# Optimization experiments

Measured on AMD Instinct MI355X. Metric: run time of the kernel, lower is better.

## Reference

```python
import jax, jax.numpy as jnp
import numpy as np

B, LI, LJ, D = 32, 512, 512, 512
NN_DIM = 256  # agg output dim = 2*NN_DIM = 512


def setup_inputs() -> dict:
    key = jax.random.key(0)
    k1, k2, k3 = jax.random.split(key, 3)
    i = jax.random.normal(k1, (B, LI, D), dtype=jnp.float32)
    j = jax.random.normal(k2, (B, LJ, D), dtype=jnp.float32)
    W_agg = jax.random.normal(k3, (D, 2 * NN_DIM), dtype=jnp.float32) * (1.0 / np.sqrt(D))
    b_agg = jnp.zeros((2 * NN_DIM,), dtype=jnp.float32)
    return {"i": i, "j": j, "W_agg": W_agg, "b_agg": b_agg}


def _agg(x, W, b):
    # shared aggregation net: Dense(2*nn_dim) + tanh, then mean-pool over time
    # x: [B, L, D] -> [B, 2*nn_dim]
    return jnp.mean(jnp.tanh(jnp.einsum('bld,dh->blh', x, W) + b), axis=1)


def reference(i, j, W_agg, b_agg):
    # cross-attention scores: [B, Li, Lj]
    weight = jnp.einsum('bik,bjk->bij', i, j)
    # row softmax (over Lj) -> weights to aggregate j per i-position
    weight_j = jax.nn.softmax(weight, axis=2)
    # column softmax (over Li) -> weights to aggregate i per j-position
    weight_i = jax.nn.softmax(weight, axis=1)
    weighted_i = jnp.einsum('bij,bid->bjd', weight_i, i)  # [B, Lj, D]
    weighted_j = jnp.einsum('bij,bjd->bid', weight_j, j)  # [B, Li, D]
    output_i = jnp.abs(i - weighted_j)  # [B, Li, D]
    output_j = jnp.abs(j - weighted_i)  # [B, Lj, D]
    oi = _agg(output_i, W_agg, b_agg)   # [B, 2*nn_dim]
    oj = _agg(output_j, W_agg, b_agg)   # [B, 2*nn_dim]
    # K.mean(K.stack([oi, oj], axis=1), axis=1)
    return 0.5 * (oi + oj)
```

## Files before the change

kernel.cpp:

```cpp
#include <hip/hip_runtime.h>
#include <math.h>

#define B_ 32
#define L_ 512
#define D_ 512
#define H_ 512

typedef unsigned short u16;
typedef _Float16 h16;
typedef h16 half8 __attribute__((ext_vector_type(8)));
typedef float f32x4 __attribute__((ext_vector_type(4)));

#define SW(r, c) ((c) ^ (((r) >> 1) & 3))

typedef __attribute__((address_space(1))) void gvoid;
typedef __attribute__((address_space(3))) void svoid;
__device__ __forceinline__ void async_cp16(const void* g, void* l) {
    __builtin_amdgcn_global_load_lds((gvoid*)g, (svoid*)l, 16, 0, 0);
}

__device__ __forceinline__ u16 f2h(float x) {
    h16 h = (h16)x;
    u16 r;
    __builtin_memcpy(&r, &h, 2);
    return r;
}
__device__ __forceinline__ float h2f(u16 u) {
    h16 h;
    __builtin_memcpy(&h, &u, 2);
    return (float)h;
}

__device__ __forceinline__ void xcd_decode(int n, int& z, int& tile) {
    int xcd = n & 7, w = n >> 3;
    z = xcd + 8 * (w >> 4);
    tile = w & 15;
}

__global__ __launch_bounds__(256) void cvt_all(const float* __restrict__ I,
                                               const float* __restrict__ Jm,
                                               const float* __restrict__ W,
                                               u16* __restrict__ Ih, u16* __restrict__ IhT,
                                               u16* __restrict__ Jh, u16* __restrict__ JhT,
                                               u16* __restrict__ WT,
                                               float* __restrict__ out) {
    const int z = blockIdx.z;
    const float* src;
    u16* h;
    u16* hT;
    size_t base;
    if (z < 32) {
        src = I; h = Ih; hT = IhT; base = (size_t)z * 512 * 512;
    } else if (z < 64) {
        src = Jm; h = Jh; hT = JhT; base = (size_t)(z - 32) * 512 * 512;
    } else {
        src = W; h = nullptr; hT = WT; base = 0;
        out[(blockIdx.y * 8 + blockIdx.x) * 256 + threadIdx.x] = 0.0f;
    }
    const int r0 = blockIdx.y * 64, c0 = blockIdx.x * 64;
    __shared__ u16 t[64][66];
    const int tid = threadIdx.x;
    const int tr = tid >> 4, tc4 = (tid & 15) * 4;
#pragma unroll
    for (int rep = 0; rep < 4; ++rep) {
        int r = rep * 16 + tr;
        f32x4 v = *(const f32x4*)(src + base + (size_t)(r0 + r) * 512 + c0 + tc4);
        unsigned h0 = f2h(v[0]), h1 = f2h(v[1]), h2 = f2h(v[2]), h3 = f2h(v[3]);
        if (h)
            *(uint2*)(h + base + (size_t)(r0 + r) * 512 + c0 + tc4) =
                make_uint2(h0 | (h1 << 16), h2 | (h3 << 16));
        t[r][tc4] = (u16)h0; t[r][tc4 + 1] = (u16)h1;
        t[r][tc4 + 2] = (u16)h2; t[r][tc4 + 3] = (u16)h3;
    }
    __syncthreads();
#pragma unroll
    for (int rep = 0; rep < 4; ++rep) {
        int r = rep * 16 + tr;
        unsigned a = t[tc4][r], b = t[tc4 + 1][r], c = t[tc4 + 2][r], d = t[tc4 + 3][r];
        *(uint2*)(hT + base + (size_t)(c0 + r) * 512 + r0 + tc4) =
            make_uint2(a | (b << 16), c | (d << 16));
    }
}

__global__ __launch_bounds__(256, 2) void score_mfma(const u16* __restrict__ Ih,
                                                     const u16* __restrict__ Jh,
                                                     u16* __restrict__ P_un,
                                                     u16* __restrict__ P_unT,
                                                     float* __restrict__ rtmax,
                                                     float* __restrict__ rtsum,
                                                     float* __restrict__ ctmax,
                                                     float* __restrict__ ctsum) {
    int b, tile;
    xcd_decode(blockIdx.x, b, tile);
    const int i0 = (tile >> 2) * 128, j0 = (tile & 3) * 128;
    __shared__ u16 Ah[128 * 32], Bh[128 * 32];
    const int tid = threadIdx.x;
    const int wave = tid >> 6, lane = tid & 63;
    const int wm = (wave >> 1) * 64, wn = (wave & 1) * 64;
    const int lr = lane & 15, q = lane >> 4;
    const size_t boff = (size_t)b * L_ * D_;
    const u16* Ibh = Ih + boff;
    const u16* Jbh = Jh + boff;

    f32x4 acc[4][4] = {};

    for (int k0 = 0; k0 < D_; k0 += 32) {
#pragma unroll
        for (int h = 0; h < 2; ++h) {
            int g = wave * 2 + h;
            int r = g * 16 + (lane >> 2);
            int cg = SW(r, lane & 3);
            async_cp16(Ibh + (size_t)(i0 + r) * D_ + k0 + cg * 8, (char*)Ah + g * 1024);
            async_cp16(Jbh + (size_t)(j0 + r) * D_ + k0 + cg * 8, (char*)Bh + g * 1024);
        }
        __syncthreads();
        half8 af[4], bf[4];
#pragma unroll
        for (int mi = 0; mi < 4; ++mi) {
            int r = wm + mi * 16 + lr;
            af[mi] = *(const half8*)&Ah[r * 32 + SW(r, q) * 8];
        }
#pragma unroll
        for (int ni = 0; ni < 4; ++ni) {
            int r = wn + ni * 16 + lr;
            bf[ni] = *(const half8*)&Bh[r * 32 + SW(r, q) * 8];
        }
#pragma unroll
        for (int mi = 0; mi < 4; ++mi)
#pragma unroll
            for (int ni = 0; ni < 4; ++ni)
                acc[mi][ni] = __builtin_amdgcn_mfma_f32_16x16x32_f16(af[mi], bf[ni], acc[mi][ni], 0, 0, 0);
        __syncthreads();
    }

    float rm[4][4];
#pragma unroll
    for (int mi = 0; mi < 4; ++mi)
#pragma unroll
        for (int r4 = 0; r4 < 4; ++r4) {
            float t = fmaxf(fmaxf(acc[mi][0][r4], acc[mi][1][r4]),
                            fmaxf(acc[mi][2][r4], acc[mi][3][r4]));
#pragma unroll
            for (int off = 1; off < 16; off <<= 1) t = fmaxf(t, __shfl_xor(t, off));
            rm[mi][r4] = t;
        }
    float cm[4];
#pragma unroll
    for (int ni = 0; ni < 4; ++ni) {
        float u = -1e30f;
#pragma unroll
        for (int mi = 0; mi < 4; ++mi)
#pragma unroll
            for (int r4 = 0; r4 < 4; ++r4) u = fmaxf(u, acc[mi][ni][r4]);
        u = fmaxf(u, __shfl_xor(u, 16));
        u = fmaxf(u, __shfl_xor(u, 32));
        cm[ni] = u;
    }

    u16* Pu_b = P_un + (size_t)b * L_ * L_;
    u16* PuT_b = P_unT + (size_t)b * L_ * L_;
    float rs[4][4] = {};
    float cs[4] = {};
#pragma unroll
    for (int mi = 0; mi < 4; ++mi)
#pragma unroll
        for (int ni = 0; ni < 4; ++ni) {
            int i_base = i0 + wm + mi * 16 + q * 4;
            int j = j0 + wn + ni * 16 + lr;
            unsigned pc[4];
#pragma unroll
            for (int r4 = 0; r4 < 4; ++r4) {
                float er = __expf(acc[mi][ni][r4] - rm[mi][r4]);
                rs[mi][r4] += er;
                Pu_b[(size_t)(i_base + r4) * L_ + j] = f2h(er);
                float ec = __expf(acc[mi][ni][r4] - cm[ni]);
                cs[ni] += ec;
                pc[r4] = f2h(ec);
            }
            *(uint2*)&PuT_b[(size_t)j * L_ + i_base] =
                make_uint2(pc[0] | (pc[1] << 16), pc[2] | (pc[3] << 16));
        }

    const int gr = (j0 + wn) >> 6;
    const int gc = (i0 + wm) >> 6;
#pragma unroll
    for (int mi = 0; mi < 4; ++mi)
#pragma unroll
        for (int r4 = 0; r4 < 4; ++r4) {
            float s = rs[mi][r4];
#pragma unroll
            for (int off = 1; off < 16; off <<= 1) s += __shfl_xor(s, off);
            if (lr == 0) {
                int i = i0 + wm + mi * 16 + q * 4 + r4;
                rtmax[((size_t)b * L_ + i) * 8 + gr] = rm[mi][r4];
                rtsum[((size_t)b * L_ + i) * 8 + gr] = s;
            }
        }
#pragma unroll
    for (int ni = 0; ni < 4; ++ni) {
        float s = cs[ni];
        s += __shfl_xor(s, 16);
        s += __shfl_xor(s, 32);
        if (q == 0) {
            int j = j0 + wn + ni * 16 + lr;
            ctmax[((size_t)b * L_ + j) * 8 + gc] = cm[ni];
            ctsum[((size_t)b * L_ + j) * 8 + gc] = s;
        }
    }
}

__global__ __launch_bounds__(256, 2) void absdiff_scaled(const u16* __restrict__ P_un,
                                                         const u16* __restrict__ P_unT,
                                                         const float* __restrict__ rtmax,
                                                         const float* __restrict__ rtsum,
                                                         const float* __restrict__ ctmax,
                                                         const float* __restrict__ ctsum,
                                                         const u16* __restrict__ JhT,
                                                         const u16* __restrict__ IhT,
                                                         const u16* __restrict__ Ih,
                                                         const u16* __restrict__ Jh,
                                                         u16* __restrict__ Xall) {
    int zz, tile;
    xcd_decode(blockIdx.x, zz, tile);
    const int side = zz >> 5, b = zz & 31;
    const int a0 = (tile >> 2) * 128, d0 = (tile & 3) * 128;
    const u16* Pb = (side ? P_unT : P_un) + (size_t)b * L_ * L_;
    const float* tmax = (side ? ctmax : rtmax) + (size_t)b * L_ * 8;
    const float* tsum = (side ? ctsum : rtsum) + (size_t)b * L_ * 8;
    const u16* Vt = (side ? IhT : JhT) + (size_t)b * D_ * L_;
    const u16* Oh = (side ? Jh : Ih) + (size_t)b * L_ * D_;
    u16* Xb = Xall + (size_t)zz * L_ * D_;

    __shared__ u16 As[128 * 32], Bs[128 * 32];
    __shared__ float sc[128][8];
    const int tid = threadIdx.x;
    const int wave = tid >> 6, lane = tid & 63;
    const int wm = (wave >> 1) * 64, wn = (wave & 1) * 64;
    const int lr = lane & 15, q = lane >> 4;

    if (tid < 128) {
        const float* tm = tmax + (size_t)(a0 + tid) * 8;
        const float* ts = tsum + (size_t)(a0 + tid) * 8;
        f32x4 m0 = *(const f32x4*)tm, m1 = *(const f32x4*)(tm + 4);
        f32x4 s0 = *(const f32x4*)ts, s1 = *(const f32x4*)(ts + 4);
        float m = fmaxf(fmaxf(fmaxf(m0[0], m0[1]), fmaxf(m0[2], m0[3])),
                        fmaxf(fmaxf(m1[0], m1[1]), fmaxf(m1[2], m1[3])));
        float e0 = __expf(m0[0] - m), e1 = __expf(m0[1] - m);
        float e2 = __expf(m0[2] - m), e3 = __expf(m0[3] - m);
        float e4 = __expf(m1[0] - m), e5 = __expf(m1[1] - m);
        float e6 = __expf(m1[2] - m), e7 = __expf(m1[3] - m);
        float inv = 1.0f / (e0 * s0[0] + e1 * s0[1] + e2 * s0[2] + e3 * s0[3] +
                            e4 * s1[0] + e5 * s1[1] + e6 * s1[2] + e7 * s1[3]);
        sc[tid][0] = e0 * inv; sc[tid][1] = e1 * inv;
        sc[tid][2] = e2 * inv; sc[tid][3] = e3 * inv;
        sc[tid][4] = e4 * inv; sc[tid][5] = e5 * inv;
        sc[tid][6] = e6 * inv; sc[tid][7] = e7 * inv;
    }
    __syncthreads();

    f32x4 acc[4][4] = {};

    for (int k0 = 0; k0 < L_; k0 += 32) {
#pragma unroll
        for (int h = 0; h < 2; ++h) {
            int g = wave * 2 + h;
            int r = g * 16 + (lane >> 2);
            int cg = SW(r, lane & 3);
            async_cp16(Pb + (size_t)(a0 + r) * L_ + k0 + cg * 8, (char*)As + g * 1024);
            async_cp16(Vt + (size_t)(d0 + r) * L_ + k0 + cg * 8, (char*)Bs + g * 1024);
        }
        __syncthreads();
        const int gk = k0 >> 6;
        half8 af[4], bf[4];
#pragma unroll
        for (int mi = 0; mi < 4; ++mi) {
            int r = wm + mi * 16 + lr;
            h16 s = (h16)sc[r][gk];
            half8 s8 = {s, s, s, s, s, s, s, s};
            af[mi] = *(const half8*)&As[r * 32 + SW(r, q) * 8] * s8;
        }
#pragma unroll
        for (int ni = 0; ni < 4; ++ni) {
            int r = wn + ni * 16 + lr;
            bf[ni] = *(const half8*)&Bs[r * 32 + SW(r, q) * 8];
        }
#pragma unroll
        for (int mi = 0; mi < 4; ++mi)
#pragma unroll
            for (int ni = 0; ni < 4; ++ni)
                acc[mi][ni] = __builtin_amdgcn_mfma_f32_16x16x32_f16(af[mi], bf[ni], acc[mi][ni], 0, 0, 0);
        __syncthreads();
    }

#pragma unroll
    for (int mi = 0; mi < 4; ++mi)
#pragma unroll
        for (int ni = 0; ni < 4; ++ni) {
            int i = a0 + wm + mi * 16 + q * 4;
            int d = d0 + wn + ni * 16 + lr;
#pragma unroll
            for (int r4 = 0; r4 < 4; ++r4) {
                float x = fabsf(h2f(Oh[(size_t)(i + r4) * D_ + d]) - acc[mi][ni][r4]);
                Xb[(size_t)(i + r4) * D_ + d] = f2h(x);
            }
        }
}

__global__ __launch_bounds__(256, 2) void agg_mfma(const u16* __restrict__ Xall,
                                                   const u16* __restrict__ Wt,
                                                   const float* __restrict__ bias,
                                                   float* __restrict__ out) {
    int zz, tile;
    xcd_decode(blockIdx.x, zz, tile);
    const int bb = zz & 31;
    const u16* Xb = Xall + (size_t)zz * L_ * D_;
    const int l0 = (tile >> 2) * 128, h0 = (tile & 3) * 128;
    __shared__ u16 As[128 * 32], Bs[128 * 32];
    const int tid = threadIdx.x;
    const int wave = tid >> 6, lane = tid & 63;
    const int wm = (wave >> 1) * 64, wn = (wave & 1) * 64;
    const int lr = lane & 15, q = lane >> 4;

    f32x4 acc[4][4] = {};

    for (int k0 = 0; k0 < D_; k0 += 32) {
#pragma unroll
        for (int h = 0; h < 2; ++h) {
            int g = wave * 2 + h;
            int r = g * 16 + (lane >> 2);
            int cg = SW(r, lane & 3);
            async_cp16(Xb + (size_t)(l0 + r) * D_ + k0 + cg * 8, (char*)As + g * 1024);
            async_cp16(Wt + (size_t)(h0 + r) * D_ + k0 + cg * 8, (char*)Bs + g * 1024);
        }
        __syncthreads();
        half8 af[4], bf[4];
#pragma unroll
        for (int mi = 0; mi < 4; ++mi) {
            int r = wm + mi * 16 + lr;
            af[mi] = *(const half8*)&As[r * 32 + SW(r, q) * 8];
        }
#pragma unroll
        for (int ni = 0; ni < 4; ++ni) {
            int r = wn + ni * 16 + lr;
            bf[ni] = *(const half8*)&Bs[r * 32 + SW(r, q) * 8];
        }
#pragma unroll
        for (int mi = 0; mi < 4; ++mi)
#pragma unroll
            for (int ni = 0; ni < 4; ++ni)
                acc[mi][ni] = __builtin_amdgcn_mfma_f32_16x16x32_f16(af[mi], bf[ni], acc[mi][ni], 0, 0, 0);
        __syncthreads();
    }

#pragma unroll
    for (int ni = 0; ni < 4; ++ni) {
        int hcol = h0 + wn + ni * 16 + lr;
        float bsv = bias[hcol];
        float ssum = 0.f;
#pragma unroll
        for (int mi = 0; mi < 4; ++mi)
#pragma unroll
            for (int r4 = 0; r4 < 4; ++r4)
                ssum += tanhf(acc[mi][ni][r4] + bsv);
        ssum += __shfl_xor(ssum, 16);
        ssum += __shfl_xor(ssum, 32);
        if (q == 0) atomicAdd(&out[bb * H_ + hcol], ssum * (0.5f / (float)L_));
    }
}

extern "C" void kernel_launch(void* const* d_in, const int* in_sizes, int n_in,
                              void* d_out, int out_size, void* d_ws, size_t ws_size,
                              hipStream_t stream) {
    const float* I = (const float*)d_in[0];
    const float* Jm = (const float*)d_in[1];
    const float* W = (const float*)d_in[2];
    const float* bias = (const float*)d_in[3];
    float* out = (float*)d_out;

    const size_t BLD = (size_t)B_ * L_ * D_;
    const size_t BLL = (size_t)B_ * L_ * L_;

    char* p = (char*)d_ws;
    auto give = [&](size_t bytes) {
        char* r = p;
        p += (bytes + 255) & ~(size_t)255;
        return r;
    };
    u16* Ih = (u16*)give(BLD * 2);
    u16* Jh = (u16*)give(BLD * 2);
    u16* IhT = (u16*)give(BLD * 2);
    u16* JhT = (u16*)give(BLD * 2);
    u16* WT = (u16*)give((size_t)D_ * H_ * 2);
    u16* P_un = (u16*)give(BLL * 2);
    u16* P_unT = (u16*)give(BLL * 2);
    float* rtmax = (float*)give((size_t)B_ * L_ * 8 * 4);
    float* rtsum = (float*)give((size_t)B_ * L_ * 8 * 4);
    float* ctmax = (float*)give((size_t)B_ * L_ * 8 * 4);
    float* ctsum = (float*)give((size_t)B_ * L_ * 8 * 4);
    u16* Xall = (u16*)give(2 * BLD * 2);

    cvt_all<<<dim3(8, 8, 65), 256, 0, stream>>>(I, Jm, W, Ih, IhT, Jh, JhT, WT, out);
    score_mfma<<<512, 256, 0, stream>>>(Ih, Jh, P_un, P_unT, rtmax, rtsum, ctmax, ctsum);
    absdiff_scaled<<<1024, 256, 0, stream>>>(P_un, P_unT, rtmax, rtsum, ctmax, ctsum,
                                             JhT, IhT, Ih, Jh, Xall);
    agg_mfma<<<1024, 256, 0, stream>>>(Xall, WT, bias, out);
}
```

Before: 194.5 us.

## Halve N-tile of absdiff and agg GEMMs to 128x64 and use fast tanh

```diff
diff --git a/kernel.cpp b/kernel.cpp
--- a/kernel.cpp
+++ b/kernel.cpp
@@ -30,11 +30,19 @@
     __builtin_memcpy(&h, &u, 2);
     return (float)h;
 }
-
-__device__ __forceinline__ void xcd_decode(int n, int& z, int& tile) {
+__device__ __forceinline__ float fast_tanh(float x) {
+    return 1.0f - 2.0f / (__expf(2.0f * x) + 1.0f);
+}
+
+__device__ __forceinline__ void xcd_decode16(int n, int& z, int& tile) {
     int xcd = n & 7, w = n >> 3;
     z = xcd + 8 * (w >> 4);
     tile = w & 15;
+}
+__device__ __forceinline__ void xcd_decode32(int n, int& z, int& tile) {
+    int xcd = n & 7, w = n >> 3;
+    z = xcd + 8 * (w >> 5);
+    tile = w & 31;
 }
 
 __global__ __launch_bounds__(256) void cvt_all(const float* __restrict__ I,
@@ -91,7 +99,7 @@
                                                      float* __restrict__ ctmax,
                                                      float* __restrict__ ctsum) {
     int b, tile;
-    xcd_decode(blockIdx.x, b, tile);
+    xcd_decode16(blockIdx.x, b, tile);
     const int i0 = (tile >> 2) * 128, j0 = (tile & 3) * 128;
     __shared__ u16 Ah[128 * 32], Bh[128 * 32];
     const int tid = threadIdx.x;
@@ -209,7 +217,7 @@
     }
 }
 
-__global__ __launch_bounds__(256, 2) void absdiff_scaled(const u16* __restrict__ P_un,
+__global__ __launch_bounds__(256, 6) void absdiff_scaled(const u16* __restrict__ P_un,
                                                          const u16* __restrict__ P_unT,
                                                          const float* __restrict__ rtmax,
                                                          const float* __restrict__ rtsum,
@@ -221,9 +229,9 @@
                                                          const u16* __restrict__ Jh,
                                                          u16* __restrict__ Xall) {
     int zz, tile;
-    xcd_decode(blockIdx.x, zz, tile);
+    xcd_decode32(blockIdx.x, zz, tile);
     const int side = zz >> 5, b = zz & 31;
-    const int a0 = (tile >> 2) * 128, d0 = (tile & 3) * 128;
+    const int a0 = (tile >> 3) * 128, d0 = (tile & 7) * 64;
     const u16* Pb = (side ? P_unT : P_un) + (size_t)b * L_ * L_;
     const float* tmax = (side ? ctmax : rtmax) + (size_t)b * L_ * 8;
     const float* tsum = (side ? ctsum : rtsum) + (size_t)b * L_ * 8;
@@ -231,11 +239,11 @@
     const u16* Oh = (side ? Jh : Ih) + (size_t)b * L_ * D_;
     u16* Xb = Xall + (size_t)zz * L_ * D_;
 
-    __shared__ u16 As[128 * 32], Bs[128 * 32];
+    __shared__ u16 As[128 * 32], Bs[64 * 32];
     __shared__ float sc[128][8];
     const int tid = threadIdx.x;
     const int wave = tid >> 6, lane = tid & 63;
-    const int wm = (wave >> 1) * 64, wn = (wave & 1) * 64;
+    const int wm = (wave >> 1) * 64, wn = (wave & 1) * 32;
     const int lr = lane & 15, q = lane >> 4;
 
     if (tid < 128) {
@@ -258,20 +266,27 @@
     }
     __syncthreads();
 
-    f32x4 acc[4][4] = {};
+    f32x4 acc[4][2] = {};
 
     for (int k0 = 0; k0 < L_; k0 += 32) {
 #pragma unroll
-        for (int h = 0; h < 2; ++h) {
-            int g = wave * 2 + h;
-            int r = g * 16 + (lane >> 2);
-            int cg = SW(r, lane & 3);
-            async_cp16(Pb + (size_t)(a0 + r) * L_ + k0 + cg * 8, (char*)As + g * 1024);
-            async_cp16(Vt + (size_t)(d0 + r) * L_ + k0 + cg * 8, (char*)Bs + g * 1024);
+        for (int gi = 0; gi < 3; ++gi) {
+            int g = wave * 3 + gi;
+            int rr = lane >> 2;
+            int cg;
+            if (g < 8) {
+                int r = g * 16 + rr;
+                cg = SW(r, lane & 3);
+                async_cp16(Pb + (size_t)(a0 + r) * L_ + k0 + cg * 8, (char*)As + g * 1024);
+            } else {
+                int r = (g - 8) * 16 + rr;
+                cg = SW(r, lane & 3);
+                async_cp16(Vt + (size_t)(d0 + r) * L_ + k0 + cg * 8, (char*)Bs + (g - 8) * 1024);
+            }
         }
         __syncthreads();
         const int gk = k0 >> 6;
-        half8 af[4], bf[4];
+        half8 af[4], bf[2];
 #pragma unroll
         for (int mi = 0; mi < 4; ++mi) {
             int r = wm + mi * 16 + lr;
@@ -280,14 +295,14 @@
             af[mi] = *(const half8*)&As[r * 32 + SW(r, q) * 8] * s8;
         }
 #pragma unroll
-        for (int ni = 0; ni < 4; ++ni) {
+        for (int ni = 0; ni < 2; ++ni) {
             int r = wn + ni * 16 + lr;
             bf[ni] = *(const half8*)&Bs[r * 32 + SW(r, q) * 8];
         }
 #pragma unroll
         for (int mi = 0; mi < 4; ++mi)
 #pragma unroll
-            for (int ni = 0; ni < 4; ++ni)
+            for (int ni = 0; ni < 2; ++ni)
                 acc[mi][ni] = __builtin_amdgcn_mfma_f32_16x16x32_f16(af[mi], bf[ni], acc[mi][ni], 0, 0, 0);
         __syncthreads();
     }
@@ -295,7 +310,7 @@
 #pragma unroll
     for (int mi = 0; mi < 4; ++mi)
 #pragma unroll
-        for (int ni = 0; ni < 4; ++ni) {
+        for (int ni = 0; ni < 2; ++ni) {
             int i = a0 + wm + mi * 16 + q * 4;
             int d = d0 + wn + ni * 16 + lr;
 #pragma unroll
@@ -306,54 +321,61 @@
         }
 }
 
-__global__ __launch_bounds__(256, 2) void agg_mfma(const u16* __restrict__ Xall,
+__global__ __launch_bounds__(256, 6) void agg_mfma(const u16* __restrict__ Xall,
                                                    const u16* __restrict__ Wt,
                                                    const float* __restrict__ bias,
                                                    float* __restrict__ out) {
     int zz, tile;
-    xcd_decode(blockIdx.x, zz, tile);
+    xcd_decode32(blockIdx.x, zz, tile);
     const int bb = zz & 31;
     const u16* Xb = Xall + (size_t)zz * L_ * D_;
-    const int l0 = (tile >> 2) * 128, h0 = (tile & 3) * 128;
-    __shared__ u16 As[128 * 32], Bs[128 * 32];
+    const int l0 = (tile >> 3) * 128, h0 = (tile & 7) * 64;
+    __shared__ u16 As[128 * 32], Bs[64 * 32];
     const int tid = threadIdx.x;
     const int wave = tid >> 6, lane = tid & 63;
-    const int wm = (wave >> 1) * 64, wn = (wave & 1) * 64;
+    const int wm = (wave >> 1) * 64, wn = (wave & 1) * 32;
     const int lr = lane & 15, q = lane >> 4;
 
-    f32x4 acc[4][4] = {};
+    f32x4 acc[4][2] = {};
 
     for (int k0 = 0; k0 < D_; k0 += 32) {
 #pragma unroll
-        for (int h = 0; h < 2; ++h) {
-            int g = wave * 2 + h;
-            int r = g * 16 + (lane >> 2);
-            int cg = SW(r, lane & 3);
-            async_cp16(Xb + (size_t)(l0 + r) * D_ + k0 + cg * 8, (char*)As + g * 1024);
-            async_cp16(Wt + (size_t)(h0 + r) * D_ + k0 + cg * 8, (char*)Bs + g * 1024);
-        }
-        __syncthreads();
-        half8 af[4], bf[4];
+        for (int gi = 0; gi < 3; ++gi) {
+            int g = wave * 3 + gi;
+            int rr = lane >> 2;
+            int cg;
+            if (g < 8) {
+                int r = g * 16 + rr;
+                cg = SW(r, lane & 3);
+                async_cp16(Xb + (size_t)(l0 + r) * D_ + k0 + cg * 8, (char*)As + g * 1024);
+            } else {
+                int r = (g - 8) * 16 + rr;
+                cg = SW(r, lane & 3);
+                async_cp16(Wt + (size_t)(h0 + r) * D_ + k0 + cg * 8, (char*)Bs + (g - 8) * 1024);
+            }
+        }
+        __syncthreads();
+        half8 af[4], bf[2];
 #pragma unroll
         for (int mi = 0; mi < 4; ++mi) {
             int r = wm + mi * 16 + lr;
             af[mi] = *(const half8*)&As[r * 32 + SW(r, q) * 8];
         }
 #pragma unroll
-        for (int ni = 0; ni < 4; ++ni) {
+        for (int ni = 0; ni < 2; ++ni) {
             int r = wn + ni * 16 + lr;
             bf[ni] = *(const half8*)&Bs[r * 32 + SW(r, q) * 8];
         }
 #pragma unroll
         for (int mi = 0; mi < 4; ++mi)
 #pragma unroll
-            for (int ni = 0; ni < 4; ++ni)
+            for (int ni = 0; ni < 2; ++ni)
                 acc[mi][ni] = __builtin_amdgcn_mfma_f32_16x16x32_f16(af[mi], bf[ni], acc[mi][ni], 0, 0, 0);
         __syncthreads();
     }
 
 #pragma unroll
-    for (int ni = 0; ni < 4; ++ni) {
+    for (int ni = 0; ni < 2; ++ni) {
         int hcol = h0 + wn + ni * 16 + lr;
         float bsv = bias[hcol];
         float ssum = 0.f;
@@ -361,7 +383,7 @@
         for (int mi = 0; mi < 4; ++mi)
 #pragma unroll
             for (int r4 = 0; r4 < 4; ++r4)
-                ssum += tanhf(acc[mi][ni][r4] + bsv);
+                ssum += fast_tanh(acc[mi][ni][r4] + bsv);
         ssum += __shfl_xor(ssum, 16);
         ssum += __shfl_xor(ssum, 32);
         if (q == 0) atomicAdd(&out[bb * H_ + hcol], ssum * (0.5f / (float)L_));
@@ -401,7 +423,7 @@
 
     cvt_all<<<dim3(8, 8, 65), 256, 0, stream>>>(I, Jm, W, Ih, IhT, Jh, JhT, WT, out);
     score_mfma<<<512, 256, 0, stream>>>(Ih, Jh, P_un, P_unT, rtmax, rtsum, ctmax, ctsum);
-    absdiff_scaled<<<1024, 256, 0, stream>>>(P_un, P_unT, rtmax, rtsum, ctmax, ctsum,
+    absdiff_scaled<<<2048, 256, 0, stream>>>(P_un, P_unT, rtmax, rtsum, ctmax, ctsum,
                                              JhT, IhT, Ih, Jh, Xall);
-    agg_mfma<<<1024, 256, 0, stream>>>(Xall, WT, bias, out);
-}
+    agg_mfma<<<2048, 256, 0, stream>>>(Xall, WT, bias, out);
+}
```

Result: slower. 206.7 us (+6.2%).
